# Kernel optimization log

Hardware: AMD Instinct MI355X
Metric: run time of the kernel (lower is better)

The kernel has to match this reference:

```python
import jax, jax.numpy as jnp
import numpy as np
import math

C_IN = 512
C = 64
N_HEAD = 8
B = 4
S = 2048


def setup_inputs() -> dict:
    key = jax.random.key(0)
    ks = jax.random.split(key, 10)
    scale = 0.02
    return {
        "x": jax.random.normal(ks[0], (B, S, C_IN), dtype=jnp.float32),
        "bias": jax.random.normal(ks[1], (N_HEAD, S, S), dtype=jnp.float32),
        "attention_mask": jax.random.randint(ks[2], (B, S), 0, 2, dtype=jnp.int32),
        "Wq": jax.random.normal(ks[3], (C * N_HEAD, C_IN), dtype=jnp.float32) * scale,
        "Wk": jax.random.normal(ks[4], (C * N_HEAD, C_IN), dtype=jnp.float32) * scale,
        "Wv": jax.random.normal(ks[5], (C * N_HEAD, C_IN), dtype=jnp.float32) * scale,
        "Wo": jax.random.normal(ks[6], (C_IN, C * N_HEAD), dtype=jnp.float32) * scale,
        "bo": jnp.zeros((C_IN,), dtype=jnp.float32),
        "Wg": jax.random.normal(ks[7], (C * N_HEAD, C_IN), dtype=jnp.float32) * scale,
        "bg": jnp.zeros((C * N_HEAD,), dtype=jnp.float32),
    }


def reference(x, bias, attention_mask, Wq, Wk, Wv, Wo, bo, Wg, bg):
    # q/k/v projections (no bias), split heads: (B,S,H*C) -> (B,H,S,C)
    def split_heads(t):
        return t.reshape(*t.shape[:-1], N_HEAD, C).swapaxes(-2, -3)

    q = split_heads(x @ Wq.T) / math.sqrt(C)
    k = split_heads(x @ Wk.T)
    v = split_heads(x @ Wv.T)

    # attention weights: (B,H,S,S)
    aw = jnp.einsum('bhqc,bhkc->bhqk', q, k)
    # bias broadcast: (H,S,S) -> (1,H,S,S)
    aw = aw + bias[None, :, :, :]
    # mask: keys with value 0 get -1e8; (B,S) -> (B,1,1,S)
    offset = (attention_mask[:, None, None, :] == 0).astype(aw.dtype) * (-1e8)
    aw = aw + offset

    scores = jax.nn.softmax(aw, axis=-1)
    attn = jnp.einsum('bhqk,bhkc->bhqc', scores, v)
    # (B,H,S,C) -> (B,S,H*C)
    attn = attn.swapaxes(-3, -2).reshape(B, S, N_HEAD * C)

    out = attn @ Wo.T + bo
    # gating applied after output layer, as in the source module
    out = jax.nn.sigmoid(out @ Wg.T + bg) * out
    return out
```

## Files before the change

### kernel.cpp

```cpp
#include <hip/hip_runtime.h>
#include <math.h>

#define Bq   4
#define Sq   2048
#define CIN  512
#define NH   8
#define CH   64
#define HC   512

typedef __attribute__((ext_vector_type(8))) short bf16x8;
typedef __attribute__((ext_vector_type(4))) float f32x4;

__device__ __forceinline__ f32x4 MFMA(bf16x8 a, bf16x8 b, f32x4 c) {
    return __builtin_amdgcn_mfma_f32_16x16x32_bf16(a, b, c, 0, 0, 0);
}

__device__ __forceinline__ void splitf(float f, unsigned short& h, unsigned short& l) {
    unsigned int u = __float_as_uint(f);
    h = (unsigned short)(u >> 16);
    float fh = __uint_as_float(u & 0xFFFF0000u);
    l = (unsigned short)(__float_as_uint(f - fh) >> 16);
}

__device__ __forceinline__ void cvt4(float4 v, ushort4& h, ushort4& l) {
    splitf(v.x, h.x, l.x); splitf(v.y, h.y, l.y);
    splitf(v.z, h.z, l.z); splitf(v.w, h.w, l.w);
}

union FRAG8 { ushort4 u4[2]; bf16x8 v; };

__global__ __launch_bounds__(256) void qkv_fused(
    const float* __restrict__ x,
    const float* __restrict__ Wq, const float* __restrict__ Wk,
    const float* __restrict__ Wv,
    float* __restrict__ Qo, float* __restrict__ Ko, float* __restrict__ Vo)
{
    __shared__ unsigned short Ah[128][72], Al[128][72];
    __shared__ unsigned short Bh[64][72],  Bl[64][72];

    const int t    = threadIdx.x;
    const int lane = t & 63;
    const int w    = t >> 6;
    const int l16  = lane & 15;
    const int g    = lane >> 4;
    const int m0   = blockIdx.x * 128;
    const int by   = blockIdx.y;
    const int sel  = by >> 3;
    const int n0   = (by & 7) * 64;
    const float* __restrict__ W = (sel == 0) ? Wq : (sel == 1) ? Wk : Wv;
    const int wm   = (w >> 1) * 64;
    const int wn   = (w & 1) * 32;
    const int srow = t >> 4;
    const int scol = (t & 15) * 4;

    const f32x4 z4 = {0.f, 0.f, 0.f, 0.f};
    f32x4 acc[4][2];
#pragma unroll
    for (int m = 0; m < 4; ++m)
#pragma unroll
        for (int n = 0; n < 2; ++n) acc[m][n] = z4;

    for (int kt = 0; kt < CIN; kt += 64) {
        __syncthreads();
#pragma unroll
        for (int s = 0; s < 8; ++s) {
            const int r = srow + s * 16;
            float4 av = *(const float4*)&x[(size_t)(m0 + r) * CIN + kt + scol];
            ushort4 h, l; cvt4(av, h, l);
            *(ushort4*)&Ah[r][scol] = h; *(ushort4*)&Al[r][scol] = l;
        }
#pragma unroll
        for (int s = 0; s < 4; ++s) {
            const int r = srow + s * 16;
            float4 bv = *(const float4*)&W[(size_t)(n0 + r) * CIN + kt + scol];
            ushort4 h, l; cvt4(bv, h, l);
            *(ushort4*)&Bh[r][scol] = h; *(ushort4*)&Bl[r][scol] = l;
        }
        __syncthreads();
#pragma unroll
        for (int kk = 0; kk < 2; ++kk) {
            const int ko = kk * 32 + g * 8;
            bf16x8 bh[2], bl[2];
#pragma unroll
            for (int n = 0; n < 2; ++n) {
                bh[n] = *(const bf16x8*)&Bh[wn + n * 16 + l16][ko];
                bl[n] = *(const bf16x8*)&Bl[wn + n * 16 + l16][ko];
            }
#pragma unroll
            for (int m = 0; m < 4; ++m) {
                bf16x8 ah = *(const bf16x8*)&Ah[wm + m * 16 + l16][ko];
                bf16x8 al = *(const bf16x8*)&Al[wm + m * 16 + l16][ko];
#pragma unroll
                for (int n = 0; n < 2; ++n) {
                    acc[m][n] = MFMA(ah, bh[n], acc[m][n]);
                    acc[m][n] = MFMA(ah, bl[n], acc[m][n]);
                    acc[m][n] = MFMA(al, bh[n], acc[m][n]);
                }
            }
        }
    }

#pragma unroll
    for (int m = 0; m < 4; ++m)
#pragma unroll
        for (int n = 0; n < 2; ++n) {
            const int col = n0 + wn + n * 16 + l16;
            const int hh  = col >> 6, d = col & 63;
#pragma unroll
            for (int r = 0; r < 4; ++r) {
                const int row = m0 + wm + m * 16 + g * 4 + r;
                const int b = row >> 11, s = row & 2047;
                float v = acc[m][n][r];
                if (sel == 0)
                    Qo[(((size_t)b * NH + hh) * Sq + s) * CH + d] = v * 0.125f;
                else if (sel == 1)
                    Ko[(((size_t)b * NH + hh) * Sq + s) * CH + d] = v;
                else
                    Vo[(((size_t)b * NH + hh) * CH + d) * Sq + s] = v;
            }
        }
}

template<int MODE>
__global__ __launch_bounds__(256) void gemm_og(
    const float* __restrict__ A, const float* __restrict__ W,
    const float* __restrict__ bias, const float* __restrict__ Oin,
    float* __restrict__ C)
{
    __shared__ unsigned short Ah[128][72], Al[128][72];
    __shared__ unsigned short Bh[64][72],  Bl[64][72];

    const int t    = threadIdx.x;
    const int lane = t & 63;
    const int w    = t >> 6;
    const int l16  = lane & 15;
    const int g    = lane >> 4;
    const int m0   = blockIdx.x * 128;
    const int n0   = blockIdx.y * 64;
    const int wm   = (w >> 1) * 64;
    const int wn   = (w & 1) * 32;
    const int srow = t >> 4;
    const int scol = (t & 15) * 4;

    const f32x4 z4 = {0.f, 0.f, 0.f, 0.f};
    f32x4 acc[4][2];
#pragma unroll
    for (int m = 0; m < 4; ++m)
#pragma unroll
        for (int n = 0; n < 2; ++n) acc[m][n] = z4;

    for (int kt = 0; kt < HC; kt += 64) {
        __syncthreads();
#pragma unroll
        for (int s = 0; s < 8; ++s) {
            const int r = srow + s * 16;
            float4 av = *(const float4*)&A[(size_t)(m0 + r) * HC + kt + scol];
            ushort4 h, l; cvt4(av, h, l);
            *(ushort4*)&Ah[r][scol] = h; *(ushort4*)&Al[r][scol] = l;
        }
#pragma unroll
        for (int s = 0; s < 4; ++s) {
            const int r = srow + s * 16;
            float4 bv = *(const float4*)&W[(size_t)(n0 + r) * HC + kt + scol];
            ushort4 h, l; cvt4(bv, h, l);
            *(ushort4*)&Bh[r][scol] = h; *(ushort4*)&Bl[r][scol] = l;
        }
        __syncthreads();
#pragma unroll
        for (int kk = 0; kk < 2; ++kk) {
            const int ko = kk * 32 + g * 8;
            bf16x8 bh[2], bl[2];
#pragma unroll
            for (int n = 0; n < 2; ++n) {
                bh[n] = *(const bf16x8*)&Bh[wn + n * 16 + l16][ko];
                bl[n] = *(const bf16x8*)&Bl[wn + n * 16 + l16][ko];
            }
#pragma unroll
            for (int m = 0; m < 4; ++m) {
                bf16x8 ah = *(const bf16x8*)&Ah[wm + m * 16 + l16][ko];
                bf16x8 al = *(const bf16x8*)&Al[wm + m * 16 + l16][ko];
#pragma unroll
                for (int n = 0; n < 2; ++n) {
                    acc[m][n] = MFMA(ah, bh[n], acc[m][n]);
                    acc[m][n] = MFMA(ah, bl[n], acc[m][n]);
                    acc[m][n] = MFMA(al, bh[n], acc[m][n]);
                }
            }
        }
    }

#pragma unroll
    for (int m = 0; m < 4; ++m)
#pragma unroll
        for (int n = 0; n < 2; ++n) {
            const int col = n0 + wn + n * 16 + l16;
#pragma unroll
            for (int r = 0; r < 4; ++r) {
                const int row = m0 + wm + m * 16 + g * 4 + r;
                float v = acc[m][n][r];
                if (MODE == 2) {
                    C[(size_t)row * HC + col] = v + bias[col];
                } else {
                    float o  = Oin[(size_t)row * HC + col];
                    float gt = 1.f / (1.f + __expf(-(v + bias[col])));
                    C[(size_t)row * HC + col] = gt * o;
                }
            }
        }
}

__global__ __launch_bounds__(256) void attn_mfma(
    const float* __restrict__ Q, const float* __restrict__ K,
    const float* __restrict__ VT, const float* __restrict__ bias,
    const int* __restrict__ mask, float* __restrict__ Aout)
{
    __shared__ unsigned short Kh[64][72], Kl[64][72];
    __shared__ unsigned short Vh[64][72], Vl[64][72];
    __shared__ __align__(16) unsigned char Pbuf[4][9216];
    __shared__ float moff[64];

    const int t    = threadIdx.x;
    const int lane = t & 63;
    const int w    = t >> 6;
    const int l16  = lane & 15;
    const int g    = lane >> 4;
    const int q0   = blockIdx.x * 128;
    const int h    = blockIdx.y;
    const int b    = blockIdx.z;
    const int wq   = w * 32;

    unsigned short* Phw = (unsigned short*)(Pbuf[w]);
    unsigned short* Plw = Phw + 32 * 72;
    float*          Bsw = (float*)(Pbuf[w]);

    const float* Qbase = Q  + (((size_t)b * NH + h) * Sq + q0 + wq) * CH;
    const float* Kbase = K  + ((size_t)b * NH + h) * Sq * CH;
    const float* Vbase = VT + ((size_t)b * NH + h) * CH * Sq;
    const float* bbase = bias + (size_t)h * Sq * Sq;

    bf16x8 qh[2][2], ql[2][2];
#pragma unroll
    for (int m = 0; m < 2; ++m)
#pragma unroll
        for (int kk = 0; kk < 2; ++kk) {
            const int row = m * 16 + l16;
            const int ko  = kk * 32 + g * 8;
            const float* p = Qbase + (size_t)row * CH + ko;
            float4 v0 = *(const float4*)p;
            float4 v1 = *(const float4*)(p + 4);
            FRAG8 fh, fl;
            cvt4(v0, fh.u4[0], fl.u4[0]);
            cvt4(v1, fh.u4[1], fl.u4[1]);
            qh[m][kk] = fh.v; ql[m][kk] = fl.v;
        }

    const f32x4 z4 = {0.f, 0.f, 0.f, 0.f};
    float m_run[2][4], l_run[2][4];
    f32x4 oacc[2][4];
#pragma unroll
    for (int m = 0; m < 2; ++m) {
#pragma unroll
        for (int r = 0; r < 4; ++r) { m_run[m][r] = -1e30f; l_run[m][r] = 0.f; }
#pragma unroll
        for (int n = 0; n < 4; ++n) oacc[m][n] = z4;
    }

    const int brow = lane >> 4;
    const int bcol = (lane & 15) * 4;

    for (int kt = 0; kt < Sq; kt += 64) {
        __syncthreads();

#pragma unroll
        for (int s = 0; s < 8; ++s) {
            const int rl = brow + s * 4;
            *(float4*)&Bsw[rl * 68 + bcol] =
                *(const float4*)&bbase[(size_t)(q0 + wq + rl) * Sq + kt + bcol];
        }

#pragma unroll
        for (int s = 0; s < 4; ++s) {
            const int rr = (t >> 4) + s * 16;
            const int cc = (t & 15) * 4;
            float4 kv = *(const float4*)&Kbase[(size_t)(kt + rr) * CH + cc];
            ushort4 hh, ll; cvt4(kv, hh, ll);
            *(ushort4*)&Kh[rr][cc] = hh; *(ushort4*)&Kl[rr][cc] = ll;
            float4 vv = *(const float4*)&Vbase[(size_t)rr * Sq + kt + cc];
            cvt4(vv, hh, ll);
            *(ushort4*)&Vh[rr][cc] = hh; *(ushort4*)&Vl[rr][cc] = ll;
        }
        if (t < 64) moff[t] = (mask[b * Sq + kt + t] == 0) ? -1e8f : 0.f;
        __syncthreads();

        f32x4 sfr[2][4];
#pragma unroll
        for (int m = 0; m < 2; ++m)
#pragma unroll
            for (int n = 0; n < 4; ++n) sfr[m][n] = z4;
#pragma unroll
        for (int kk = 0; kk < 2; ++kk) {
            const int ko = kk * 32 + g * 8;
            bf16x8 kh[4], kl[4];
#pragma unroll
            for (int n = 0; n < 4; ++n) {
                kh[n] = *(const bf16x8*)&Kh[n * 16 + l16][ko];
                kl[n] = *(const bf16x8*)&Kl[n * 16 + l16][ko];
            }
#pragma unroll
            for (int m = 0; m < 2; ++m)
#pragma unroll
                for (int n = 0; n < 4; ++n) {
                    sfr[m][n] = MFMA(qh[m][kk], kh[n], sfr[m][n]);
                    sfr[m][n] = MFMA(qh[m][kk], kl[n], sfr[m][n]);
                    sfr[m][n] = MFMA(ql[m][kk], kh[n], sfr[m][n]);
                }
        }

#pragma unroll
        for (int m = 0; m < 2; ++m)
#pragma unroll
            for (int n = 0; n < 4; ++n) {
                const int colk = n * 16 + l16;
                const float mo = moff[colk];
#pragma unroll
                for (int r = 0; r < 4; ++r)
                    sfr[m][n][r] += Bsw[(m * 16 + g * 4 + r) * 68 + colk] + mo;
            }

        asm volatile("" ::: "memory");

#pragma unroll
        for (int m = 0; m < 2; ++m) {
#pragma unroll
            for (int r = 0; r < 4; ++r) {
                float mx = fmaxf(fmaxf(sfr[m][0][r], sfr[m][1][r]),
                                 fmaxf(sfr[m][2][r], sfr[m][3][r]));
                mx = fmaxf(mx, __shfl_xor(mx, 1));
                mx = fmaxf(mx, __shfl_xor(mx, 2));
                mx = fmaxf(mx, __shfl_xor(mx, 4));
                mx = fmaxf(mx, __shfl_xor(mx, 8));
                const float newm = fmaxf(m_run[m][r], mx);
                const float corr = __expf(m_run[m][r] - newm);
                m_run[m][r] = newm;
                float rs = 0.f;
#pragma unroll
                for (int n = 0; n < 4; ++n) {
                    float p = __expf(sfr[m][n][r] - newm);
                    sfr[m][n][r] = p;
                    rs += p;
                }
                rs += __shfl_xor(rs, 1);
                rs += __shfl_xor(rs, 2);
                rs += __shfl_xor(rs, 4);
                rs += __shfl_xor(rs, 8);
                l_run[m][r] = l_run[m][r] * corr + rs;
#pragma unroll
                for (int n = 0; n < 4; ++n) oacc[m][n][r] *= corr;
                const int prl = m * 16 + g * 4 + r;
#pragma unroll
                for (int n = 0; n < 4; ++n) {
                    unsigned short hh, ll;
                    splitf(sfr[m][n][r], hh, ll);
                    Phw[prl * 72 + n * 16 + l16] = hh;
                    Plw[prl * 72 + n * 16 + l16] = ll;
                }
            }
        }

#pragma unroll
        for (int kk = 0; kk < 2; ++kk) {
            const int ko = kk * 32 + g * 8;
            bf16x8 vh[4], vl[4];
#pragma unroll
            for (int n = 0; n < 4; ++n) {
                vh[n] = *(const bf16x8*)&Vh[n * 16 + l16][ko];
                vl[n] = *(const bf16x8*)&Vl[n * 16 + l16][ko];
            }
#pragma unroll
            for (int m = 0; m < 2; ++m) {
                bf16x8 ph = *(const bf16x8*)&Phw[(m * 16 + l16) * 72 + ko];
                bf16x8 pl = *(const bf16x8*)&Plw[(m * 16 + l16) * 72 + ko];
#pragma unroll
                for (int n = 0; n < 4; ++n) {
                    oacc[m][n] = MFMA(ph, vh[n], oacc[m][n]);
                    oacc[m][n] = MFMA(ph, vl[n], oacc[m][n]);
                    oacc[m][n] = MFMA(pl, vh[n], oacc[m][n]);
                }
            }
        }
    }

#pragma unroll
    for (int m = 0; m < 2; ++m)
#pragma unroll
        for (int r = 0; r < 4; ++r) {
            const float inv = 1.f / l_run[m][r];
            const int row = q0 + wq + m * 16 + g * 4 + r;
#pragma unroll
            for (int n = 0; n < 4; ++n)
                Aout[((size_t)b * Sq + row) * HC + h * CH + n * 16 + l16] =
                    oacc[m][n][r] * inv;
        }
}

extern "C" void kernel_launch(void* const* d_in, const int* in_sizes, int n_in,
                              void* d_out, int out_size, void* d_ws, size_t ws_size,
                              hipStream_t stream)
{
    const float* x    = (const float*)d_in[0];
    const float* bias = (const float*)d_in[1];
    const int*   mask = (const int*)d_in[2];
    const float* Wq   = (const float*)d_in[3];
    const float* Wk   = (const float*)d_in[4];
    const float* Wv   = (const float*)d_in[5];
    const float* Wo   = (const float*)d_in[6];
    const float* bo   = (const float*)d_in[7];
    const float* Wg   = (const float*)d_in[8];
    const float* bg   = (const float*)d_in[9];
    float* out = (float*)d_out;
    float* ws  = (float*)d_ws;

    const size_t QS = (size_t)Bq * NH * Sq * CH;
    float* Q    = ws;
    float* Kt   = ws + QS;
    float* VT   = ws + 2 * QS;
    float* attn = ws + 3 * QS;
    float* O    = Q;

    qkv_fused<<<dim3(64, 24), 256, 0, stream>>>(x, Wq, Wk, Wv, Q, Kt, VT);

    attn_mfma<<<dim3(Sq / 128, NH, Bq), 256, 0, stream>>>(Q, Kt, VT, bias, mask, attn);

    gemm_og<2><<<dim3(64, 8), 256, 0, stream>>>(attn, Wo, bo, nullptr, O);
    gemm_og<3><<<dim3(64, 8), 256, 0, stream>>>(O,    Wg, bg, O,       out);
}
```

Before: 486.6 us.

## Pre-split weights and intermediates into bf16 hi/lo once, swizzle P buffer

Adds a prep kernel that splits all five weight matrices into bf16 hi/lo pairs once per call. K, V^T and the output projection are written already split by their producer kernels, so attention and the gate GEMM load ushort data straight into shared memory with no per-tile conversion. This removes repeated fp32-to-bf16 split work, since each K/V tile is otherwise re-converted by every query block. The P scratch buffer in attention gets an XOR column swizzle to cut LDS bank conflicts. The cost is one extra launch and more workspace.

```diff
diff --git a/kernel.cpp b/kernel.cpp
--- a/kernel.cpp
+++ b/kernel.cpp
@@ -27,13 +27,33 @@
     splitf(v.z, h.z, l.z); splitf(v.w, h.w, l.w);
 }
 
+__device__ __forceinline__ int pswz(int row, int col) {
+    return col ^ (((row >> 2) & 7) << 3);
+}
+
 union FRAG8 { ushort4 u4[2]; bf16x8 v; };
 
+__global__ __launch_bounds__(256) void prep_split(
+    const float* __restrict__ Wq, const float* __restrict__ Wk,
+    const float* __restrict__ Wv, const float* __restrict__ Wo,
+    const float* __restrict__ Wg, unsigned short* __restrict__ dst)
+{
+    const int y = blockIdx.y;
+    const float* __restrict__ src =
+        (y == 0) ? Wq : (y == 1) ? Wk : (y == 2) ? Wv : (y == 3) ? Wo : Wg;
+    unsigned short* __restrict__ h = dst + (size_t)y * 2 * (HC * CIN);
+    unsigned short* __restrict__ l = h + HC * CIN;
+    const int i = (blockIdx.x * 256 + threadIdx.x) * 4;
+    float4 v = *(const float4*)&src[i];
+    ushort4 hh, ll; cvt4(v, hh, ll);
+    *(ushort4*)&h[i] = hh; *(ushort4*)&l[i] = ll;
+}
+
 __global__ __launch_bounds__(256) void qkv_fused(
-    const float* __restrict__ x,
-    const float* __restrict__ Wq, const float* __restrict__ Wk,
-    const float* __restrict__ Wv,
-    float* __restrict__ Qo, float* __restrict__ Ko, float* __restrict__ Vo)
+    const float* __restrict__ x, const unsigned short* __restrict__ Wsp,
+    float* __restrict__ Qo,
+    unsigned short* __restrict__ Khi, unsigned short* __restrict__ Klo,
+    unsigned short* __restrict__ VThi, unsigned short* __restrict__ VTlo)
 {
     __shared__ unsigned short Ah[128][72], Al[128][72];
     __shared__ unsigned short Bh[64][72],  Bl[64][72];
@@ -47,7 +67,8 @@
     const int by   = blockIdx.y;
     const int sel  = by >> 3;
     const int n0   = (by & 7) * 64;
-    const float* __restrict__ W = (sel == 0) ? Wq : (sel == 1) ? Wk : Wv;
+    const unsigned short* __restrict__ Wh = Wsp + (size_t)sel * 2 * (HC * CIN);
+    const unsigned short* __restrict__ Wl = Wh + HC * CIN;
     const int wm   = (w >> 1) * 64;
     const int wn   = (w & 1) * 32;
     const int srow = t >> 4;
@@ -72,9 +93,8 @@
 #pragma unroll
         for (int s = 0; s < 4; ++s) {
             const int r = srow + s * 16;
-            float4 bv = *(const float4*)&W[(size_t)(n0 + r) * CIN + kt + scol];
-            ushort4 h, l; cvt4(bv, h, l);
-            *(ushort4*)&Bh[r][scol] = h; *(ushort4*)&Bl[r][scol] = l;
+            *(ushort4*)&Bh[r][scol] = *(const ushort4*)&Wh[(size_t)(n0 + r) * CIN + kt + scol];
+            *(ushort4*)&Bl[r][scol] = *(const ushort4*)&Wl[(size_t)(n0 + r) * CIN + kt + scol];
         }
         __syncthreads();
 #pragma unroll
@@ -111,21 +131,29 @@
                 const int row = m0 + wm + m * 16 + g * 4 + r;
                 const int b = row >> 11, s = row & 2047;
                 float v = acc[m][n][r];
-                if (sel == 0)
+                if (sel == 0) {
                     Qo[(((size_t)b * NH + hh) * Sq + s) * CH + d] = v * 0.125f;
-                else if (sel == 1)
-                    Ko[(((size_t)b * NH + hh) * Sq + s) * CH + d] = v;
-                else
-                    Vo[(((size_t)b * NH + hh) * CH + d) * Sq + s] = v;
+                } else if (sel == 1) {
+                    unsigned short vh, vl; splitf(v, vh, vl);
+                    const size_t idx = (((size_t)b * NH + hh) * Sq + s) * CH + d;
+                    Khi[idx] = vh; Klo[idx] = vl;
+                } else {
+                    unsigned short vh, vl; splitf(v, vh, vl);
+                    const size_t idx = (((size_t)b * NH + hh) * CH + d) * Sq + s;
+                    VThi[idx] = vh; VTlo[idx] = vl;
+                }
             }
         }
 }
 
 template<int MODE>
 __global__ __launch_bounds__(256) void gemm_og(
-    const float* __restrict__ A, const float* __restrict__ W,
-    const float* __restrict__ bias, const float* __restrict__ Oin,
-    float* __restrict__ C)
+    const float* __restrict__ Af,
+    const unsigned short* __restrict__ Ah_g, const unsigned short* __restrict__ Al_g,
+    const unsigned short* __restrict__ Wh_g, const unsigned short* __restrict__ Wl_g,
+    const float* __restrict__ bias,
+    unsigned short* __restrict__ OutH, unsigned short* __restrict__ OutL,
+    float* __restrict__ Cout)
 {
     __shared__ unsigned short Ah[128][72], Al[128][72];
     __shared__ unsigned short Bh[64][72],  Bl[64][72];
@@ -154,16 +182,20 @@
 #pragma unroll
         for (int s = 0; s < 8; ++s) {
             const int r = srow + s * 16;
-            float4 av = *(const float4*)&A[(size_t)(m0 + r) * HC + kt + scol];
-            ushort4 h, l; cvt4(av, h, l);
-            *(ushort4*)&Ah[r][scol] = h; *(ushort4*)&Al[r][scol] = l;
+            if (MODE == 2) {
+                float4 av = *(const float4*)&Af[(size_t)(m0 + r) * HC + kt + scol];
+                ushort4 h, l; cvt4(av, h, l);
+                *(ushort4*)&Ah[r][scol] = h; *(ushort4*)&Al[r][scol] = l;
+            } else {
+                *(ushort4*)&Ah[r][scol] = *(const ushort4*)&Ah_g[(size_t)(m0 + r) * HC + kt + scol];
+                *(ushort4*)&Al[r][scol] = *(const ushort4*)&Al_g[(size_t)(m0 + r) * HC + kt + scol];
+            }
         }
 #pragma unroll
         for (int s = 0; s < 4; ++s) {
             const int r = srow + s * 16;
-            float4 bv = *(const float4*)&W[(size_t)(n0 + r) * HC + kt + scol];
-            ushort4 h, l; cvt4(bv, h, l);
-            *(ushort4*)&Bh[r][scol] = h; *(ushort4*)&Bl[r][scol] = l;
+            *(ushort4*)&Bh[r][scol] = *(const ushort4*)&Wh_g[(size_t)(n0 + r) * HC + kt + scol];
+            *(ushort4*)&Bl[r][scol] = *(const ushort4*)&Wl_g[(size_t)(n0 + r) * HC + kt + scol];
         }
         __syncthreads();
 #pragma unroll
@@ -197,22 +229,28 @@
 #pragma unroll
             for (int r = 0; r < 4; ++r) {
                 const int row = m0 + wm + m * 16 + g * 4 + r;
-                float v = acc[m][n][r];
+                const float v = acc[m][n][r] + bias[col];
                 if (MODE == 2) {
-                    C[(size_t)row * HC + col] = v + bias[col];
+                    unsigned short vh, vl; splitf(v, vh, vl);
+                    OutH[(size_t)row * HC + col] = vh;
+                    OutL[(size_t)row * HC + col] = vl;
                 } else {
-                    float o  = Oin[(size_t)row * HC + col];
-                    float gt = 1.f / (1.f + __expf(-(v + bias[col])));
-                    C[(size_t)row * HC + col] = gt * o;
+                    float oh = __uint_as_float((unsigned)Ah_g[(size_t)row * HC + col] << 16);
+                    float ol = __uint_as_float((unsigned)Al_g[(size_t)row * HC + col] << 16);
+                    const float o = oh + ol;
+                    const float gt = 1.f / (1.f + __expf(-v));
+                    Cout[(size_t)row * HC + col] = gt * o;
                 }
             }
         }
 }
 
 __global__ __launch_bounds__(256) void attn_mfma(
-    const float* __restrict__ Q, const float* __restrict__ K,
-    const float* __restrict__ VT, const float* __restrict__ bias,
-    const int* __restrict__ mask, float* __restrict__ Aout)
+    const float* __restrict__ Q,
+    const unsigned short* __restrict__ KhiG, const unsigned short* __restrict__ KloG,
+    const unsigned short* __restrict__ VhiG, const unsigned short* __restrict__ VloG,
+    const float* __restrict__ bias, const int* __restrict__ mask,
+    float* __restrict__ Aout)
 {
     __shared__ unsigned short Kh[64][72], Kl[64][72];
     __shared__ unsigned short Vh[64][72], Vl[64][72];
@@ -233,10 +271,12 @@
     unsigned short* Plw = Phw + 32 * 72;
     float*          Bsw = (float*)(Pbuf[w]);
 
-    const float* Qbase = Q  + (((size_t)b * NH + h) * Sq + q0 + wq) * CH;
-    const float* Kbase = K  + ((size_t)b * NH + h) * Sq * CH;
-    const float* Vbase = VT + ((size_t)b * NH + h) * CH * Sq;
-    const float* bbase = bias + (size_t)h * Sq * Sq;
+    const float*          Qbase = Q    + (((size_t)b * NH + h) * Sq + q0 + wq) * CH;
+    const unsigned short* KhB   = KhiG + ((size_t)b * NH + h) * Sq * CH;
+    const unsigned short* KlB   = KloG + ((size_t)b * NH + h) * Sq * CH;
+    const unsigned short* VhB   = VhiG + ((size_t)b * NH + h) * CH * Sq;
+    const unsigned short* VlB   = VloG + ((size_t)b * NH + h) * CH * Sq;
+    const float*          bbase = bias + (size_t)h * Sq * Sq;
 
     bf16x8 qh[2][2], ql[2][2];
 #pragma unroll
@@ -282,12 +322,10 @@
         for (int s = 0; s < 4; ++s) {
             const int rr = (t >> 4) + s * 16;
             const int cc = (t & 15) * 4;
-            float4 kv = *(const float4*)&Kbase[(size_t)(kt + rr) * CH + cc];
-            ushort4 hh, ll; cvt4(kv, hh, ll);
-            *(ushort4*)&Kh[rr][cc] = hh; *(ushort4*)&Kl[rr][cc] = ll;
-            float4 vv = *(const float4*)&Vbase[(size_t)rr * Sq + kt + cc];
-            cvt4(vv, hh, ll);
-            *(ushort4*)&Vh[rr][cc] = hh; *(ushort4*)&Vl[rr][cc] = ll;
+            *(ushort4*)&Kh[rr][cc] = *(const ushort4*)&KhB[(size_t)(kt + rr) * CH + cc];
+            *(ushort4*)&Kl[rr][cc] = *(const ushort4*)&KlB[(size_t)(kt + rr) * CH + cc];
+            *(ushort4*)&Vh[rr][cc] = *(const ushort4*)&VhB[(size_t)rr * Sq + kt + cc];
+            *(ushort4*)&Vl[rr][cc] = *(const ushort4*)&VlB[(size_t)rr * Sq + kt + cc];
         }
         if (t < 64) moff[t] = (mask[b * Sq + kt + t] == 0) ? -1e8f : 0.f;
         __syncthreads();
@@ -361,8 +399,9 @@
                 for (int n = 0; n < 4; ++n) {
                     unsigned short hh, ll;
                     splitf(sfr[m][n][r], hh, ll);
-                    Phw[prl * 72 + n * 16 + l16] = hh;
-                    Plw[prl * 72 + n * 16 + l16] = ll;
+                    const int pc = pswz(prl, n * 16 + l16);
+                    Phw[prl * 72 + pc] = hh;
+                    Plw[prl * 72 + pc] = ll;
                 }
             }
         }
@@ -378,8 +417,10 @@
             }
 #pragma unroll
             for (int m = 0; m < 2; ++m) {
-                bf16x8 ph = *(const bf16x8*)&Phw[(m * 16 + l16) * 72 + ko];
-                bf16x8 pl = *(const bf16x8*)&Plw[(m * 16 + l16) * 72 + ko];
+                const int prow = m * 16 + l16;
+                const int pko  = ko ^ (((prow >> 2) & 7) << 3);
+                bf16x8 ph = *(const bf16x8*)&Phw[prow * 72 + pko];
+                bf16x8 pl = *(const bf16x8*)&Plw[prow * 72 + pko];
 #pragma unroll
                 for (int n = 0; n < 4; ++n) {
                     oacc[m][n] = MFMA(ph, vh[n], oacc[m][n]);
@@ -421,16 +462,31 @@
     float* ws  = (float*)d_ws;
 
     const size_t QS = (size_t)Bq * NH * Sq * CH;
-    float* Q    = ws;
-    float* Kt   = ws + QS;
-    float* VT   = ws + 2 * QS;
-    float* attn = ws + 3 * QS;
-    float* O    = Q;
-
-    qkv_fused<<<dim3(64, 24), 256, 0, stream>>>(x, Wq, Wk, Wv, Q, Kt, VT);
-
-    attn_mfma<<<dim3(Sq / 128, NH, Bq), 256, 0, stream>>>(Q, Kt, VT, bias, mask, attn);
-
-    gemm_og<2><<<dim3(64, 8), 256, 0, stream>>>(attn, Wo, bo, nullptr, O);
-    gemm_og<3><<<dim3(64, 8), 256, 0, stream>>>(O,    Wg, bg, O,       out);
-}
+
+    float*          Q    = ws;
+    unsigned short* Khi  = (unsigned short*)(ws + QS);
+    unsigned short* Klo  = Khi + QS;
+    unsigned short* VThi = (unsigned short*)(ws + 2 * QS);
+    unsigned short* VTlo = VThi + QS;
+    float*          attn = ws + 3 * QS;
+    unsigned short* Wsp  = (unsigned short*)(ws + 4 * QS);
+    unsigned short* Ohi  = (unsigned short*)Q;
+    unsigned short* Olo  = Ohi + QS;
+
+    const unsigned short* Woh = Wsp + (size_t)3 * 2 * (HC * CIN);
+    const unsigned short* Wol = Woh + HC * CIN;
+    const unsigned short* Wgh = Wsp + (size_t)4 * 2 * (HC * CIN);
+    const unsigned short* Wgl = Wgh + HC * CIN;
+
+    prep_split<<<dim3(256, 5), 256, 0, stream>>>(Wq, Wk, Wv, Wo, Wg, Wsp);
+
+    qkv_fused<<<dim3(64, 24), 256, 0, stream>>>(x, Wsp, Q, Khi, Klo, VThi, VTlo);
+
+    attn_mfma<<<dim3(Sq / 128, NH, Bq), 256, 0, stream>>>(
+        Q, Khi, Klo, VThi, VTlo, bias, mask, attn);
+
+    gemm_og<2><<<dim3(64, 8), 256, 0, stream>>>(
+        attn, nullptr, nullptr, Woh, Wol, bo, Ohi, Olo, nullptr);
+    gemm_og<3><<<dim3(64, 8), 256, 0, stream>>>(
+        nullptr, Ohi, Olo, Wgh, Wgl, bg, nullptr, nullptr, out);
+}
```

Result: slower. 975.9 us (+100.6%).
